# Performance work log

Hardware: AMD Instinct MI355X
Metric: run time of the kernel (lower is better)

The kernel has to match this reference:

```python
import jax, jax.numpy as jnp
import numpy as np

NUM_CODES = 1024
CODE_DIM = 256
COMMIT_W = 0.25
EPS = 1e-5
ENT_LO, ENT_HI = 0.5, 0.9
ENT_W = 0.1
VAR_FLOOR = 0.05
VAR_W = 1e-3
DECORR_W = 1e-3


def setup_inputs() -> dict:
    key = jax.random.key(0)
    k1, k2, k3 = jax.random.split(key, 3)
    inputs = jax.random.normal(k1, (16, 2048, CODE_DIM), dtype=jnp.float32)
    weight = jax.random.normal(k2, (NUM_CODES, CODE_DIM), dtype=jnp.float32) * 0.1
    usage_counts = jax.random.uniform(k3, (NUM_CODES,), dtype=jnp.float32)
    return {"inputs": inputs, "weight": weight, "usage_counts": usage_counts}


def reference(inputs, weight, usage_counts):
    K, D = weight.shape
    flat = inputs.reshape(-1, D)  # [N, D]
    # squared euclidean distances [N, K]
    dist = (flat ** 2).sum(axis=1, keepdims=True) - 2.0 * flat @ weight.T + (weight ** 2).sum(axis=1)
    idx = jnp.argmin(dist, axis=1)  # [N]
    quant = weight[idx].reshape(inputs.shape)

    commitment_loss = COMMIT_W * jnp.mean((jax.lax.stop_gradient(quant) - inputs) ** 2)
    # straight-through estimator
    quant_ste = inputs + jax.lax.stop_gradient(quant - inputs)

    # usage entropy regularizer
    probs = usage_counts + EPS
    probs = probs / jnp.maximum(probs.sum(), EPS * K)
    usage_entropy = -jnp.sum(probs * jnp.log(probs + EPS)) / np.log(float(K)).astype(np.float32)
    gap = jnp.where(usage_entropy < ENT_LO, ENT_LO - usage_entropy,
                    jnp.where(usage_entropy > ENT_HI, usage_entropy - ENT_HI, 0.0))
    entropy_loss = ENT_W * gap ** 2

    # variance floor penalty on codebook
    variance = jnp.var(weight, axis=0)
    variance_loss = VAR_W * jnp.mean(jax.nn.relu(VAR_FLOOR - variance))

    # decorrelation penalty
    wc = weight - weight.mean(axis=0, keepdims=True)
    cov = wc.T @ wc / float(K)  # [D, D]
    off_diag = cov - jnp.diag(jnp.diag(cov))
    decorrelation_loss = DECORR_W * jnp.mean(off_diag ** 2)

    total_loss = commitment_loss + entropy_loss + variance_loss + decorrelation_loss
    indices = idx.reshape(inputs.shape[:-1])
    return (quant_ste, indices, total_loss, commitment_loss, entropy_loss,
            variance_loss, decorrelation_loss, usage_entropy)
```

## Files before the change

### kernel.cpp

```cpp
#include <hip/hip_runtime.h>
#include <math.h>

#define DIMS   256
#define KCODES 1024
#define NTOT   32768
#define TAU    4.0e-4f

typedef __bf16 bf16x8 __attribute__((ext_vector_type(8)));
typedef float  f32x4  __attribute__((ext_vector_type(4)));

#define WS_COMMIT   0
#define WS_FLAGCNT  1
#define WS_DECORR   2
#define WS_COLSUM   16
#define WS_COLSQ    272
#define WS_WSQ      1024
#define WS_XSQ      2048
#define WS_FLAGS    34816
#define WS_CAND1    67584
#define WS_CAND2    329728
#define WS_CANDI    591872
#define WS_WP       854016

#define OUT_Q    0
#define OUT_IDX  8388608
#define OUT_SCAL 8421376


__global__ __launch_bounds__(256) void prep_kernel(const float* __restrict__ X,
                                                   const float* __restrict__ W,
                                                   __bf16* __restrict__ Xp,
                                                   __bf16* __restrict__ Wp2,
                                                   float* ws) {
  int b = blockIdx.x;
  int tid = threadIdx.x;
  if (b < 1056) {
    __shared__ float sqred[256];
    bool isW = b >= 1024;
    const float* src = isW ? W : X;
    __bf16* dst = isW ? Wp2 : Xp;
    int sqoff = isW ? WS_WSQ : WS_XSQ;
    int bb = isW ? b - 1024 : b;
    int kt = tid >> 5, mtl = (tid >> 4) & 1, lc = tid & 15;
    int row = bb * 32 + mtl * 16 + lc;
    int bt = row >> 7, c = row & 127;
    int wv = c >> 6, t = (c >> 4) & 3;
    size_t hibase = ((((size_t)(bt * 8 + kt) * 2 + wv) * 4 + t) * 2) * 512;
    const float* s = src + (size_t)row * DIMS + kt * 32;
    float sq = 0.f;
    #pragma unroll
    for (int kq = 0; kq < 4; kq++) {
      float4 u = *(const float4*)(s + kq * 8);
      float4 v = *(const float4*)(s + kq * 8 + 4);
      float f[8] = {u.x, u.y, u.z, u.w, v.x, v.y, v.z, v.w};
      bf16x8 hi, lo;
      #pragma unroll
      for (int e = 0; e < 8; e++) {
        __bf16 h = (__bf16)f[e];
        hi[e] = h;
        lo[e] = (__bf16)(f[e] - (float)h);
        sq = fmaf(f[e], f[e], sq);
      }
      size_t off = (size_t)(kq * 16 + lc) * 8;
      *(bf16x8*)&dst[hibase + off] = hi;
      *(bf16x8*)&dst[hibase + 512 + off] = lo;
    }
    sqred[tid] = sq;
    __syncthreads();
    if (tid < 32) {
      float s8 = 0.f;
      #pragma unroll
      for (int k = 0; k < 8; k++) s8 += sqred[k * 32 + tid];
      ws[sqoff + bb * 32 + tid] = s8;
    }
  } else {
    __shared__ float wi_s[KCODES];
    __shared__ float red2[256];
    __shared__ float miB;
    __shared__ float red[4];
    int i0 = b - 1056;
    #pragma unroll
    for (int q = 0; q < 4; q++) {
      int row = q * 256 + tid;
      wi_s[row] = W[(size_t)row * DIMS + i0];
    }
    __syncthreads();
    float pm = 0.f;
    #pragma unroll
    for (int q = 0; q < 4; q++) pm += wi_s[tid * 4 + q];
    red2[tid] = pm;
    __syncthreads();
    if (tid == 0) {
      float s = 0.f;
      for (int k = 0; k < 256; k++) s += red2[k];
      miB = s * (1.0f / 1024.0f);
    }
    int j = tid;
    float a0 = 0.f, sj = 0.f, sqj = 0.f;
    for (int k = 0; k < KCODES; k += 4) {
      #pragma unroll
      for (int u = 0; u < 4; u++) {
        float wj = W[(size_t)(k + u) * DIMS + j];
        a0 = fmaf(wi_s[k + u], wj, a0);
        sj += wj;
        sqj = fmaf(wj, wj, sqj);
      }
    }
    if (j == i0) {
      ws[WS_COLSUM + i0] = sj;
      ws[WS_COLSQ + i0] = sqj;
    }
    __syncthreads();
    const float inv = 1.0f / 1024.0f;
    float mj = sj * inv;
    float v = 0.f;
    float c0 = a0 * inv - miB * mj;
    if (i0 != j) v = c0 * c0;
    #pragma unroll
    for (int m = 32; m >= 1; m >>= 1) v += __shfl_xor(v, m);
    if ((j & 63) == 0) red[j >> 6] = v;
    __syncthreads();
    if (j == 0) atomicAdd(&ws[WS_DECORR], (red[0] + red[1]) + (red[2] + red[3]));
  }
}

__device__ __forceinline__ void stage16(const __bf16* g, __bf16* l) {
  __builtin_amdgcn_global_load_lds(
      (const __attribute__((address_space(1))) void*)g,
      (__attribute__((address_space(3))) void*)l, 16, 0, 0);
}

__global__ __launch_bounds__(256, 3) void pass1_kernel(const __bf16* __restrict__ Xp,
                                                       const __bf16* __restrict__ Wp2,
                                                       float* ws) {
  __shared__ __align__(16) __bf16 buf[16384];
  __shared__ float wsqs[128];
  __shared__ float d1L[256];
  __shared__ float d2L[256];
  __shared__ int   i1L[256];

  int tid = threadIdx.x;
  int lane = tid & 63, wave = tid >> 6;
  int wm = wave >> 1, wn = wave & 1;
  int quad = lane >> 4, col = lane & 15;
  int l = blockIdx.x;
  int x = l & 7;
  int j = l >> 3;
  int bm = x * 32 + (j & 15) + (j >> 7) * 16;
  int bn = (j >> 4) & 7;
  int rowBase = bm * 128, cb = bn * 128;

  if (tid < 128) wsqs[tid] = ws[WS_WSQ + cb + tid];

  f32x4 acc[4][4];
  #pragma unroll
  for (int i = 0; i < 4; i++)
    #pragma unroll
    for (int jj = 0; jj < 4; jj++) acc[i][jj] = (f32x4){0.f, 0.f, 0.f, 0.f};

  const __bf16* aSrc = Xp + (size_t)bm * 65536;
  const __bf16* bSrc = Wp2 + (size_t)bn * 65536;

  #pragma unroll
  for (int kt = 0; kt < 8; kt++) {
    __syncthreads();
    #pragma unroll
    for (int q = 0; q < 4; q++) {
      stage16(aSrc + kt * 8192 + q * 2048 + tid * 8, buf + q * 2048 + tid * 8);
      stage16(bSrc + kt * 8192 + q * 2048 + tid * 8, buf + 8192 + q * 2048 + tid * 8);
    }
    __syncthreads();

    const __bf16* bA = buf + wm * 4096 + lane * 8;
    const __bf16* bB = buf + 8192 + wn * 4096 + lane * 8;
    bf16x8 Bf[4][2];
    #pragma unroll
    for (int nt = 0; nt < 4; nt++) {
      Bf[nt][0] = *(const bf16x8*)(bB + nt * 1024);
      Bf[nt][1] = *(const bf16x8*)(bB + nt * 1024 + 512);
    }
    #pragma unroll
    for (int mt = 0; mt < 4; mt++) {
      bf16x8 A0 = *(const bf16x8*)(bA + mt * 1024);
      bf16x8 A1 = *(const bf16x8*)(bA + mt * 1024 + 512);
      #pragma unroll
      for (int nt = 0; nt < 4; nt++) {
        acc[mt][nt] = __builtin_amdgcn_mfma_f32_16x16x32_bf16(A0, Bf[nt][0], acc[mt][nt], 0, 0, 0);
        acc[mt][nt] = __builtin_amdgcn_mfma_f32_16x16x32_bf16(A0, Bf[nt][1], acc[mt][nt], 0, 0, 0);
        acc[mt][nt] = __builtin_amdgcn_mfma_f32_16x16x32_bf16(A1, Bf[nt][0], acc[mt][nt], 0, 0, 0);
      }
    }
  }
  __syncthreads();

  #pragma unroll
  for (int mt = 0; mt < 4; mt++) {
    #pragma unroll
    for (int r = 0; r < 4; r++) {
      float d1 = 3.0e38f, d2 = 3.0e38f;
      int i1 = 0;
      #pragma unroll
      for (int nt = 0; nt < 4; nt++) {
        int lc = wn * 64 + nt * 16 + col;
        float d = wsqs[lc] - 2.0f * acc[mt][nt][r];
        int g = cb + lc;
        if (d < d1) { d2 = d1; d1 = d; i1 = g; }
        else if (d < d2) d2 = d;
      }
      #pragma unroll
      for (int m = 1; m < 16; m <<= 1) {
        float od1 = __shfl_xor(d1, m);
        int oi1 = __shfl_xor(i1, m);
        float od2 = __shfl_xor(d2, m);
        if (od1 < d1 || (od1 == d1 && oi1 < i1)) {
          d2 = fminf(d1, fminf(d2, od2));
          d1 = od1; i1 = oi1;
        } else {
          d2 = fminf(od1, fminf(d2, od2));
        }
      }
      if (col == 0) {
        int lr = wm * 64 + mt * 16 + quad * 4 + r;
        d1L[lr * 2 + wn] = d1;
        d2L[lr * 2 + wn] = d2;
        i1L[lr * 2 + wn] = i1;
      }
    }
  }
  __syncthreads();
  if (tid < 128) {
    float a1 = d1L[tid * 2], a2 = d2L[tid * 2];
    int ai = i1L[tid * 2];
    float b1 = d1L[tid * 2 + 1], b2 = d2L[tid * 2 + 1];
    int bi = i1L[tid * 2 + 1];
    float m1, m2; int mi;
    if (b1 < a1 || (b1 == a1 && bi < ai)) { m1 = b1; mi = bi; m2 = fminf(a1, b2); }
    else { m1 = a1; mi = ai; m2 = fminf(b1, a2); }
    int o = bn * NTOT + rowBase + tid;
    ws[WS_CAND1 + o] = m1;
    ws[WS_CAND2 + o] = m2;
    ((int*)ws)[WS_CANDI + o] = mi;
  }
}

__global__ __launch_bounds__(256) void pass2_kernel(const float* __restrict__ W,
                                                    float* __restrict__ outQ,
                                                    float* __restrict__ outIdx, float* ws) {
  __shared__ float p1L[4][64];
  __shared__ float p2L[4][64];
  __shared__ int   piL[4][64];
  __shared__ int   idx_s[64];
  int tid = threadIdx.x;
  int r0 = blockIdx.x * 64;
  int grp = tid >> 6, rl = tid & 63;
  int row = r0 + rl;
  const float* c1 = ws + WS_CAND1;
  const float* c2 = ws + WS_CAND2;
  const int* ci = (const int*)ws + WS_CANDI;
  {
    int oa = (2 * grp) * NTOT + row;
    int ob = (2 * grp + 1) * NTOT + row;
    float a1 = c1[oa], a2 = c2[oa];
    int ai = ci[oa];
    float b1 = c1[ob], b2 = c2[ob];
    int bi = ci[ob];
    float m1, m2; int mi;
    if (b1 < a1 || (b1 == a1 && bi < ai)) { m1 = b1; mi = bi; m2 = fminf(a1, b2); }
    else { m1 = a1; mi = ai; m2 = fminf(a2, b1); }
    p1L[grp][rl] = m1;
    p2L[grp][rl] = m2;
    piL[grp][rl] = mi;
  }
  __syncthreads();
  if (tid < 64) {
    float m1 = p1L[0][tid], m2 = p2L[0][tid];
    int mi = piL[0][tid];
    #pragma unroll
    for (int w = 1; w < 4; w++) {
      float b1 = p1L[w][tid], b2 = p2L[w][tid];
      int bi = piL[w][tid];
      if (b1 < m1 || (b1 == m1 && bi < mi)) { m2 = fminf(m1, b2); m1 = b1; mi = bi; }
      else { m2 = fminf(m2, b1); }
    }
    int rw = r0 + tid;
    outIdx[rw] = (float)mi;
    idx_s[tid] = mi;
    int* wsI = (int*)ws;
    if (m2 - m1 < TAU) {
      int p = atomicAdd(&wsI[WS_FLAGCNT], 1);
      wsI[WS_FLAGS + p] = rw;
    }
    float partial = ws[WS_XSQ + rw] + m1;
    #pragma unroll
    for (int m = 32; m >= 1; m >>= 1) partial += __shfl_xor(partial, m);
    if (tid == 0) atomicAdd(&ws[WS_COMMIT], partial);
  }
  __syncthreads();
  int wave = tid >> 6, lane = tid & 63;
  #pragma unroll 4
  for (int i = 0; i < 16; i++) {
    int rr = wave * 16 + i;
    int ix = idx_s[rr];
    float4 v = ((const float4*)(W + (size_t)ix * DIMS))[lane];
    ((float4*)(outQ + (size_t)(r0 + rr) * DIMS))[lane] = v;
  }
}

__global__ __launch_bounds__(256) void refine_kernel(const float* __restrict__ X,
                                                     const float* __restrict__ W,
                                                     float* __restrict__ outQ,
                                                     float* __restrict__ outIdx, float* ws,
                                                     const float* __restrict__ U,
                                                     float* __restrict__ out) {
  __shared__ float xs[DIMS];
  __shared__ double dm[256];
  __shared__ int im[256];
  __shared__ int chosen;
  int tid = threadIdx.x;
  if (blockIdx.x == 512) {
    __shared__ float red[256];
    float s = 0.f;
    for (int e = tid; e < KCODES; e += 256) s += U[e] + 1e-5f;
    red[tid] = s;
    __syncthreads();
    for (int st = 128; st >= 1; st >>= 1) {
      if (tid < st) red[tid] += red[tid + st];
      __syncthreads();
    }
    float S = red[0];
    __syncthreads();
    float denom = fmaxf(S, 1e-5f * 1024.0f);
    float h = 0.f;
    for (int e = tid; e < KCODES; e += 256) {
      float p = (U[e] + 1e-5f) / denom;
      h += p * logf(p + 1e-5f);
    }
    red[tid] = h;
    __syncthreads();
    for (int st = 128; st >= 1; st >>= 1) {
      if (tid < st) red[tid] += red[tid + st];
      __syncthreads();
    }
    float H = -red[0] / 6.93147180559945f;
    __syncthreads();
    float m = ws[WS_COLSUM + tid] * (1.0f / 1024.0f);
    float var = ws[WS_COLSQ + tid] * (1.0f / 1024.0f) - m * m;
    float r = 0.05f - var;
    red[tid] = r > 0.f ? r : 0.f;
    __syncthreads();
    for (int st = 128; st >= 1; st >>= 1) {
      if (tid < st) red[tid] += red[tid + st];
      __syncthreads();
    }
    if (tid == 0) {
      float varloss = 1e-3f * (red[0] / 256.0f);
      float gap = H < 0.5f ? (0.5f - H) : (H > 0.9f ? (H - 0.9f) : 0.0f);
      float entloss = 0.1f * gap * gap;
      float commit = 0.25f * ws[WS_COMMIT] / 8388608.0f;
      float dec = 1e-3f * ws[WS_DECORR] / 65536.0f;
      float* sc = out + OUT_SCAL;
      sc[0] = commit + entloss + varloss + dec;
      sc[1] = commit;
      sc[2] = entloss;
      sc[3] = varloss;
      sc[4] = dec;
      sc[5] = H;
    }
    return;
  }
  const int* wsI = (const int*)ws;
  int cnt = wsI[WS_FLAGCNT];
  const int* list = wsI + WS_FLAGS;
  for (int f = blockIdx.x; f < cnt; f += 512) {
    int row = list[f];
    __syncthreads();
    if (tid < 64) ((float4*)xs)[tid] = ((const float4*)(X + (size_t)row * DIMS))[tid];
    __syncthreads();
    double bd = 1.0e300;
    int bi = 0;
    for (int jj = 0; jj < 4; jj++) {
      int c = tid + 256 * jj;
      double a0 = 0.0, a1 = 0.0, a2 = 0.0, a3 = 0.0;
      const float* wr = W + (size_t)c * DIMS;
      #pragma unroll 4
      for (int d4 = 0; d4 < 64; d4++) {
        float4 w = ((const float4*)wr)[d4];
        float4 x = ((const float4*)xs)[d4];
        double e0 = (double)x.x - (double)w.x;
        double e1 = (double)x.y - (double)w.y;
        double e2 = (double)x.z - (double)w.z;
        double e3 = (double)x.w - (double)w.w;
        a0 += e0 * e0; a1 += e1 * e1; a2 += e2 * e2; a3 += e3 * e3;
      }
      double s = (a0 + a1) + (a2 + a3);
      if (s < bd) { bd = s; bi = c; }
    }
    dm[tid] = bd; im[tid] = bi;
    __syncthreads();
    for (int st = 128; st >= 1; st >>= 1) {
      if (tid < st) {
        if (dm[tid + st] < dm[tid] || (dm[tid + st] == dm[tid] && im[tid + st] < im[tid])) {
          dm[tid] = dm[tid + st]; im[tid] = im[tid + st];
        }
      }
      __syncthreads();
    }
    if (tid == 0) { chosen = im[0]; outIdx[row] = (float)im[0]; }
    __syncthreads();
    int ix = chosen;
    if (tid < 64)
      ((float4*)(outQ + (size_t)row * DIMS))[tid] = ((const float4*)(W + (size_t)ix * DIMS))[tid];
  }
}

extern "C" void kernel_launch(void* const* d_in, const int* in_sizes, int n_in, void* d_out,
                              int out_size, void* d_ws, size_t ws_size, hipStream_t stream) {
  const float* X = (const float*)d_in[0];
  const float* W = (const float*)d_in[1];
  const float* U = (const float*)d_in[2];
  float* out = (float*)d_out;
  float* ws = (float*)d_ws;
  __bf16* Xp = (__bf16*)(out + OUT_Q);
  __bf16* Wp2 = (__bf16*)(ws + WS_WP);

  hipMemsetAsync(d_ws, 0, 12, stream);
  prep_kernel<<<1312, 256, 0, stream>>>(X, W, Xp, Wp2, ws);
  pass1_kernel<<<2048, 256, 0, stream>>>(Xp, Wp2, ws);
  pass2_kernel<<<512, 256, 0, stream>>>(W, out + OUT_Q, out + OUT_IDX, ws);
  refine_kernel<<<513, 256, 0, stream>>>(X, W, out + OUT_Q, out + OUT_IDX, ws, U, out);
}
```

Before: 236.3 us.

## Retile distance GEMM to 256x256 blocks with double-buffered LDS prefetch

```diff
diff --git a/kernel.cpp b/kernel.cpp
--- a/kernel.cpp
+++ b/kernel.cpp
@@ -130,71 +130,98 @@
       (__attribute__((address_space(3))) void*)l, 16, 0, 0);
 }
 
-__global__ __launch_bounds__(256, 3) void pass1_kernel(const __bf16* __restrict__ Xp,
+#define STAGE_PIECE(T, J) do {                                                      \
+    __bf16* _d = buf + ((T) & 1) * 32768;                                           \
+    if ((J) < 4) {                                                                  \
+      int _c = (J) >> 1, _h = (J) & 1;                                              \
+      stage16(Xp + (size_t)(bm * 2 + _c) * 65536 + (size_t)(T) * 8192 + _h * 4096 + tid * 8, \
+              _d + _c * 8192 + _h * 4096 + tid * 8);                                \
+    } else {                                                                        \
+      int _c = ((J) - 4) >> 1, _h = (J) & 1;                                        \
+      stage16(Wp2 + (size_t)(bn * 2 + _c) * 65536 + (size_t)(T) * 8192 + _h * 4096 + tid * 8, \
+              _d + 16384 + _c * 8192 + _h * 4096 + tid * 8);                        \
+    }                                                                               \
+  } while (0)
+
+__global__ __launch_bounds__(512, 1) void pass1_kernel(const __bf16* __restrict__ Xp,
                                                        const __bf16* __restrict__ Wp2,
                                                        float* ws) {
-  __shared__ __align__(16) __bf16 buf[16384];
-  __shared__ float wsqs[128];
-  __shared__ float d1L[256];
-  __shared__ float d2L[256];
-  __shared__ int   i1L[256];
+  __shared__ __align__(16) __bf16 buf[65536];
+  __shared__ float wsqs[256];
+  __shared__ float d1L[256][4];
+  __shared__ float d2L[256][4];
+  __shared__ int   i1L[256][4];
 
   int tid = threadIdx.x;
   int lane = tid & 63, wave = tid >> 6;
-  int wm = wave >> 1, wn = wave & 1;
+  int wm = wave >> 2, wn = wave & 3;
   int quad = lane >> 4, col = lane & 15;
   int l = blockIdx.x;
   int x = l & 7;
   int j = l >> 3;
-  int bm = x * 32 + (j & 15) + (j >> 7) * 16;
-  int bn = (j >> 4) & 7;
-  int rowBase = bm * 128, cb = bn * 128;
-
-  if (tid < 128) wsqs[tid] = ws[WS_WSQ + cb + tid];
-
-  f32x4 acc[4][4];
+  int bm = x * 16 + (j & 7) + (j >> 5) * 8;
+  int bn = (j >> 3) & 3;
+  int cb = bn * 256;
+
+  f32x4 acc[8][4];
   #pragma unroll
-  for (int i = 0; i < 4; i++)
+  for (int i = 0; i < 8; i++)
     #pragma unroll
     for (int jj = 0; jj < 4; jj++) acc[i][jj] = (f32x4){0.f, 0.f, 0.f, 0.f};
 
-  const __bf16* aSrc = Xp + (size_t)bm * 65536;
-  const __bf16* bSrc = Wp2 + (size_t)bn * 65536;
+  wsqs[tid & 255] = ws[WS_WSQ + cb + (tid & 255)];
+
+  STAGE_PIECE(0, 0); STAGE_PIECE(0, 1); STAGE_PIECE(0, 2); STAGE_PIECE(0, 3);
+  STAGE_PIECE(0, 4); STAGE_PIECE(0, 5); STAGE_PIECE(0, 6); STAGE_PIECE(0, 7);
+  asm volatile("s_waitcnt vmcnt(0)" ::: "memory");
+  __builtin_amdgcn_s_barrier();
+
+  #pragma unroll 2
+  for (int kt = 0; kt < 8; kt++) {
+    const __bf16* sl = buf + (kt & 1) * 32768;
+    const __bf16* bA = sl + wm * 8192 + lane * 8;
+    const __bf16* bB = sl + 16384 + (wn >> 1) * 8192 + (wn & 1) * 4096 + lane * 8;
+    bf16x8 Bf[4][2];
+    #pragma unroll
+    for (int p = 0; p < 4; p++) {
+      if (p == 0) {
+        #pragma unroll
+        for (int nt = 0; nt < 4; nt++) {
+          Bf[nt][0] = *(const bf16x8*)(bB + nt * 1024);
+          Bf[nt][1] = *(const bf16x8*)(bB + nt * 1024 + 512);
+        }
+      }
+      bf16x8 A0a = *(const bf16x8*)(bA + (2 * p + 0) * 1024);
+      bf16x8 A0b = *(const bf16x8*)(bA + (2 * p + 0) * 1024 + 512);
+      bf16x8 A1a = *(const bf16x8*)(bA + (2 * p + 1) * 1024);
+      bf16x8 A1b = *(const bf16x8*)(bA + (2 * p + 1) * 1024 + 512);
+      if (kt < 7) {
+        if (p == 0) { STAGE_PIECE(kt + 1, 0); STAGE_PIECE(kt + 1, 1);
+                      STAGE_PIECE(kt + 1, 2); STAGE_PIECE(kt + 1, 3); }
+        if (p == 1) { STAGE_PIECE(kt + 1, 4); STAGE_PIECE(kt + 1, 5);
+                      STAGE_PIECE(kt + 1, 6); STAGE_PIECE(kt + 1, 7); }
+      }
+      __builtin_amdgcn_s_barrier();
+      asm volatile("s_waitcnt lgkmcnt(0)" ::: "memory");
+      __builtin_amdgcn_sched_barrier(0);
+      __builtin_amdgcn_s_setprio(1);
+      #pragma unroll
+      for (int nt = 0; nt < 4; nt++) {
+        acc[2 * p + 0][nt] = __builtin_amdgcn_mfma_f32_16x16x32_bf16(A0a, Bf[nt][0], acc[2 * p + 0][nt], 0, 0, 0);
+        acc[2 * p + 0][nt] = __builtin_amdgcn_mfma_f32_16x16x32_bf16(A0a, Bf[nt][1], acc[2 * p + 0][nt], 0, 0, 0);
+        acc[2 * p + 0][nt] = __builtin_amdgcn_mfma_f32_16x16x32_bf16(A0b, Bf[nt][0], acc[2 * p + 0][nt], 0, 0, 0);
+        acc[2 * p + 1][nt] = __builtin_amdgcn_mfma_f32_16x16x32_bf16(A1a, Bf[nt][0], acc[2 * p + 1][nt], 0, 0, 0);
+        acc[2 * p + 1][nt] = __builtin_amdgcn_mfma_f32_16x16x32_bf16(A1a, Bf[nt][1], acc[2 * p + 1][nt], 0, 0, 0);
+        acc[2 * p + 1][nt] = __builtin_amdgcn_mfma_f32_16x16x32_bf16(A1b, Bf[nt][0], acc[2 * p + 1][nt], 0, 0, 0);
+      }
+      __builtin_amdgcn_s_setprio(0);
+      if (p == 3 && kt < 7) asm volatile("s_waitcnt vmcnt(0)" ::: "memory");
+      __builtin_amdgcn_s_barrier();
+    }
+  }
 
   #pragma unroll
-  for (int kt = 0; kt < 8; kt++) {
-    __syncthreads();
-    #pragma unroll
-    for (int q = 0; q < 4; q++) {
-      stage16(aSrc + kt * 8192 + q * 2048 + tid * 8, buf + q * 2048 + tid * 8);
-      stage16(bSrc + kt * 8192 + q * 2048 + tid * 8, buf + 8192 + q * 2048 + tid * 8);
-    }
-    __syncthreads();
-
-    const __bf16* bA = buf + wm * 4096 + lane * 8;
-    const __bf16* bB = buf + 8192 + wn * 4096 + lane * 8;
-    bf16x8 Bf[4][2];
-    #pragma unroll
-    for (int nt = 0; nt < 4; nt++) {
-      Bf[nt][0] = *(const bf16x8*)(bB + nt * 1024);
-      Bf[nt][1] = *(const bf16x8*)(bB + nt * 1024 + 512);
-    }
-    #pragma unroll
-    for (int mt = 0; mt < 4; mt++) {
-      bf16x8 A0 = *(const bf16x8*)(bA + mt * 1024);
-      bf16x8 A1 = *(const bf16x8*)(bA + mt * 1024 + 512);
-      #pragma unroll
-      for (int nt = 0; nt < 4; nt++) {
-        acc[mt][nt] = __builtin_amdgcn_mfma_f32_16x16x32_bf16(A0, Bf[nt][0], acc[mt][nt], 0, 0, 0);
-        acc[mt][nt] = __builtin_amdgcn_mfma_f32_16x16x32_bf16(A0, Bf[nt][1], acc[mt][nt], 0, 0, 0);
-        acc[mt][nt] = __builtin_amdgcn_mfma_f32_16x16x32_bf16(A1, Bf[nt][0], acc[mt][nt], 0, 0, 0);
-      }
-    }
-  }
-  __syncthreads();
-
-  #pragma unroll
-  for (int mt = 0; mt < 4; mt++) {
+  for (int mt = 0; mt < 8; mt++) {
     #pragma unroll
     for (int r = 0; r < 4; r++) {
       float d1 = 3.0e38f, d2 = 3.0e38f;
@@ -220,23 +247,25 @@
         }
       }
       if (col == 0) {
-        int lr = wm * 64 + mt * 16 + quad * 4 + r;
-        d1L[lr * 2 + wn] = d1;
-        d2L[lr * 2 + wn] = d2;
-        i1L[lr * 2 + wn] = i1;
+        int lr = wm * 128 + mt * 16 + quad * 4 + r;
+        d1L[lr][wn] = d1;
+        d2L[lr][wn] = d2;
+        i1L[lr][wn] = i1;
       }
     }
   }
   __syncthreads();
-  if (tid < 128) {
-    float a1 = d1L[tid * 2], a2 = d2L[tid * 2];
-    int ai = i1L[tid * 2];
-    float b1 = d1L[tid * 2 + 1], b2 = d2L[tid * 2 + 1];
-    int bi = i1L[tid * 2 + 1];
-    float m1, m2; int mi;
-    if (b1 < a1 || (b1 == a1 && bi < ai)) { m1 = b1; mi = bi; m2 = fminf(a1, b2); }
-    else { m1 = a1; mi = ai; m2 = fminf(b1, a2); }
-    int o = bn * NTOT + rowBase + tid;
+  if (tid < 256) {
+    float m1 = d1L[tid][0], m2 = d2L[tid][0];
+    int mi = i1L[tid][0];
+    #pragma unroll
+    for (int w = 1; w < 4; w++) {
+      float b1 = d1L[tid][w], b2 = d2L[tid][w];
+      int bi = i1L[tid][w];
+      if (b1 < m1 || (b1 == m1 && bi < mi)) { m2 = fminf(m1, b2); m1 = b1; mi = bi; }
+      else { m2 = fminf(m2, fminf(b1, b2)); }
+    }
+    int o = bn * NTOT + bm * 256 + tid;
     ws[WS_CAND1 + o] = m1;
     ws[WS_CAND2 + o] = m2;
     ((int*)ws)[WS_CANDI + o] = mi;
@@ -276,7 +305,7 @@
     float m1 = p1L[0][tid], m2 = p2L[0][tid];
     int mi = piL[0][tid];
     #pragma unroll
-    for (int w = 1; w < 4; w++) {
+    for (int w = 1; w < 2; w++) {
       float b1 = p1L[w][tid], b2 = p2L[w][tid];
       int bi = piL[w][tid];
       if (b1 < m1 || (b1 == m1 && bi < mi)) { m2 = fminf(m1, b2); m1 = b1; mi = bi; }
@@ -425,7 +454,7 @@
 
   hipMemsetAsync(d_ws, 0, 12, stream);
   prep_kernel<<<1312, 256, 0, stream>>>(X, W, Xp, Wp2, ws);
-  pass1_kernel<<<2048, 256, 0, stream>>>(Xp, Wp2, ws);
+  pass1_kernel<<<512, 512, 0, stream>>>(Xp, Wp2, ws);
   pass2_kernel<<<512, 256, 0, stream>>>(W, out + OUT_Q, out + OUT_IDX, ws);
   refine_kernel<<<513, 256, 0, stream>>>(X, W, out + OUT_Q, out + OUT_IDX, ws, U, out);
 }
```

New measurement: 239.1 us. No clear change (+1.2%).
